# Optimization experiments

Hardware: AMD Instinct MI355X
Metric: run time of the kernel (lower is better)

## Reference

```python
import jax, jax.numpy as jnp
import numpy as np

NUM_USERS = 50000
NUM_ITEMS = 10000
NUM_SUPPORT = 5
INPUT_DIM = 512
OUTPUT_DIM = 500
NNZ = 400000


def setup_inputs() -> dict:
    key = jax.random.key(0)
    ks = jax.random.split(key, 6)
    x_u = jax.random.normal(ks[0], (NUM_USERS, INPUT_DIM), dtype=jnp.float32)
    x_v = jax.random.normal(ks[1], (NUM_ITEMS, INPUT_DIM), dtype=jnp.float32)
    # random-uniform-like weight init (weight_variable_random_uniform)
    weights_u = jax.random.normal(ks[2], (INPUT_DIM, OUTPUT_DIM), dtype=jnp.float32) * 0.05
    sup_vals = jax.random.uniform(ks[3], (NUM_SUPPORT, NNZ), dtype=jnp.float32)
    sup_rows = jax.random.randint(ks[4], (NUM_SUPPORT, NNZ), 0, NUM_USERS, dtype=jnp.int32)
    sup_cols = jax.random.randint(ks[5], (NUM_SUPPORT, NNZ), 0, NUM_ITEMS, dtype=jnp.int32)
    return {"x_u": x_u, "x_v": x_v, "weights_u": weights_u,
            "sup_vals": sup_vals, "sup_rows": sup_rows, "sup_cols": sup_cols}


def reference(x_u, x_v, weights_u, sup_vals, sup_rows, sup_cols):
    # share_user_item_weights=True -> weights_v is weights_u; dropout=0.0 -> identity.
    hidden = OUTPUT_DIM // NUM_SUPPORT  # 100
    supports_u, supports_v = [], []
    for i in range(NUM_SUPPORT):
        Wi = jax.lax.dynamic_slice_in_dim(weights_u, i * hidden, hidden, axis=1)
        tmp_u = x_u @ Wi  # [num_users, hidden]
        tmp_v = x_v @ Wi  # [num_items, hidden]
        vals = sup_vals[i][:, None]  # [nnz, 1]
        rows, cols = sup_rows[i], sup_cols[i]
        # support_i @ tmp_v  (sparse [U,I] times dense [I,h])
        su = jax.ops.segment_sum(vals * tmp_v[cols], rows, num_segments=NUM_USERS)
        # support_i^T @ tmp_u (sparse [I,U] times dense [U,h])
        sv = jax.ops.segment_sum(vals * tmp_u[rows], cols, num_segments=NUM_ITEMS)
        supports_u.append(su)
        supports_v.append(sv)
    z_u = jnp.concatenate(supports_u, axis=1)  # [num_users, output_dim]
    z_v = jnp.concatenate(supports_v, axis=1)  # [num_items, output_dim]
    return (jax.nn.relu(z_u), jax.nn.relu(z_v))
```

## Files before the change

### kernel.cpp

```cpp
#include <hip/hip_runtime.h>

#define NUM_USERS   50000
#define NUM_ITEMS   10000
#define NUM_SUPPORT 5
#define INPUT_DIM   512
#define OUTPUT_DIM  500
#define NPAD        512
#define HIDDEN      100
#define HPAD        128
#define NNZ         400000
#define NEDGE       (NUM_SUPPORT * NNZ)

#define CH_E        8192
#define NCHUNK      ((NEDGE + CH_E - 1) / CH_E)
#define NB_U        ((NUM_SUPPORT * NUM_USERS + 255) / 256)
#define NB_V        ((NUM_SUPPORT * NUM_ITEMS + 255) / 256)
#define HISTM_U_SZ  (NB_U * NCHUNK)
#define HISTM_U_ALIGN 239616
#define HISTM_V_SZ  (NB_V * NCHUNK)
#define HISTM_TOT   (HISTM_U_ALIGN + HISTM_V_SZ)

typedef unsigned int u32;
typedef unsigned short ushort_t;
typedef __attribute__((ext_vector_type(4))) float f32x4;
typedef __attribute__((ext_vector_type(8))) short bf16x8;

#define GLDS(g, l) __builtin_amdgcn_global_load_lds( \
    (const __attribute__((address_space(1))) unsigned int*)(g), \
    (__attribute__((address_space(3))) unsigned int*)(l), 16, 0, 0)

__device__ inline ushort_t bf16_rne(float f) {
    u32 u = __float_as_uint(f);
    u32 r = (u + 0x7FFFu + ((u >> 16) & 1u)) >> 16;
    return (ushort_t)r;
}
__device__ inline float bf16_lo_f32(u32 w) { return __uint_as_float(w << 16); }
__device__ inline float bf16_hi_f32(u32 w) { return __uint_as_float(w & 0xFFFF0000u); }

__global__ __launch_bounds__(256) void cvt_bf16_2(
    const float4* __restrict__ a, const float4* __restrict__ b,
    ushort4* __restrict__ oa, ushort4* __restrict__ ob, int na4, int nb4)
{
    int t = blockIdx.x * 256 + threadIdx.x;
    const float4* src;
    ushort4* dst;
    int idx;
    if (t < na4) { src = a; dst = oa; idx = t; }
    else { idx = t - na4; if (idx >= nb4) return; src = b; dst = ob; }
    float4 v = src[idx];
    ushort4 o;
    o.x = bf16_rne(v.x); o.y = bf16_rne(v.y);
    o.z = bf16_rne(v.z); o.w = bf16_rne(v.w);
    dst[idx] = o;
}

__global__ __launch_bounds__(256) void make_WbT(
    const float* __restrict__ W, ushort_t* __restrict__ WbT)
{
    int t = blockIdx.x * 256 + threadIdx.x;
    int n = t >> 9, k = t & 511;
    float v = (n < OUTPUT_DIM) ? W[k * OUTPUT_DIM + n] : 0.f;
    WbT[t] = bf16_rne(v);
}

#define BM 128
#define BN 128
#define BK 32

__global__ __launch_bounds__(256) void gemm_mfma_bf16(
    const ushort_t* __restrict__ A,
    const ushort_t* __restrict__ BT,
    ushort_t* __restrict__ Xp,
    int M)
{
    const int K = INPUT_DIM;
    __shared__ ushort_t As[BM * BK];
    __shared__ ushort_t Bs[BN * BK];

    const int tid  = threadIdx.x;
    const int wave = tid >> 6;
    const int lane = tid & 63;
    const int quad = lane >> 4;
    const int lr   = lane & 15;
    const int m0 = blockIdx.x * BM;
    const int n0 = blockIdx.y * BN;
    const int wm = (wave >> 1) * 64;
    const int wn = (wave & 1) * 64;

    f32x4 acc[4][4] = {};

    for (int k0 = 0; k0 < K; k0 += BK) {
        #pragma unroll
        for (int h = 0; h < 2; ++h) {
            int o   = tid * 16 + h * 4096;
            int row = o >> 6;
            int byt = o & 63;
            int gr  = m0 + row; if (gr >= M) gr = M - 1;
            GLDS((const char*)A + ((long long)gr * K + k0) * 2 + byt, (char*)As + o);
        }
        #pragma unroll
        for (int h = 0; h < 2; ++h) {
            int o   = tid * 16 + h * 4096;
            int row = o >> 6;
            int byt = o & 63;
            GLDS((const char*)BT + ((long long)(n0 + row) * K + k0) * 2 + byt, (char*)Bs + o);
        }
        asm volatile("s_waitcnt vmcnt(0)" ::: "memory");
        __syncthreads();

        bf16x8 af[4], bfr[4];
        #pragma unroll
        for (int tm = 0; tm < 4; ++tm)
            af[tm] = *(const bf16x8*)(As + (wm + tm * 16 + lr) * BK + quad * 8);
        #pragma unroll
        for (int tn = 0; tn < 4; ++tn)
            bfr[tn] = *(const bf16x8*)(Bs + (wn + tn * 16 + lr) * BK + quad * 8);
        #pragma unroll
        for (int tm = 0; tm < 4; ++tm)
            #pragma unroll
            for (int tn = 0; tn < 4; ++tn)
                acc[tm][tn] = __builtin_amdgcn_mfma_f32_16x16x32_bf16(
                    af[tm], bfr[tn], acc[tm][tn], 0, 0, 0);
        __syncthreads();
    }

    #pragma unroll
    for (int tm = 0; tm < 4; ++tm) {
        int rbase = m0 + wm + tm * 16 + quad * 4;
        #pragma unroll
        for (int tn = 0; tn < 4; ++tn) {
            int col = n0 + wn + tn * 16 + lr;
            if (col >= OUTPUT_DIM) continue;
            int seg = col / HIDDEN;
            int off = col - seg * HIDDEN;
            ushort_t* dst = Xp + (long long)seg * M * HPAD + off;
            #pragma unroll
            for (int g = 0; g < 4; ++g) {
                int row = rbase + g;
                if (row < M) dst[(long long)row * HPAD] = bf16_rne(acc[tm][tn][g]);
            }
        }
    }
}

__global__ __launch_bounds__(256) void scan1(u32* __restrict__ data, int n,
                                             u32* __restrict__ partials)
{
    __shared__ u32 sh[256];
    int t = threadIdx.x;
    int base = blockIdx.x * 1024 + t * 4;
    u32 x[4];
    #pragma unroll
    for (int k = 0; k < 4; ++k) {
        int idx = base + k;
        x[k] = (idx < n) ? data[idx] : 0u;
    }
    u32 tsum = x[0] + x[1] + x[2] + x[3];
    sh[t] = tsum;
    __syncthreads();
    for (int off = 1; off < 256; off <<= 1) {
        u32 v = (t >= off) ? sh[t - off] : 0u;
        __syncthreads();
        sh[t] += v;
        __syncthreads();
    }
    u32 run = (t > 0) ? sh[t - 1] : 0u;
    if (t == 255) partials[blockIdx.x] = sh[255];
    #pragma unroll
    for (int k = 0; k < 4; ++k) {
        int idx = base + k;
        if (idx < n) data[idx] = run;
        run += x[k];
    }
}

__global__ __launch_bounds__(512) void scan_partials(u32* __restrict__ partials, int n)
{
    __shared__ u32 sh[512];
    int t = threadIdx.x;
    u32 x = (t < n) ? partials[t] : 0u;
    sh[t] = x;
    __syncthreads();
    for (int off = 1; off < 512; off <<= 1) {
        u32 v = (t >= off) ? sh[t - off] : 0u;
        __syncthreads();
        sh[t] += v;
        __syncthreads();
    }
    if (t < n) partials[t] = (t > 0) ? sh[t - 1] : 0u;
}

__global__ __launch_bounds__(256) void scan_add(u32* __restrict__ data, int n,
                                                const u32* __restrict__ partials)
{
    int idx = blockIdx.x * 256 + threadIdx.x;
    if (idx >= n) return;
    u32 adj = (idx >= HISTM_U_ALIGN) ? (u32)NEDGE : 0u;
    data[idx] = data[idx] + partials[idx >> 10] - adj;
}

__global__ __launch_bounds__(256) void hist_uv(
    const int* __restrict__ rows, const int* __restrict__ cols,
    u32* __restrict__ histm_u, u32* __restrict__ histm_v)
{
    __shared__ u32 hu[NB_U];
    __shared__ u32 hv[NB_V];
    const int tid = threadIdx.x;
    const int c = blockIdx.x;
    if (c == 0)
        for (int z = HISTM_U_SZ + tid; z < HISTM_U_ALIGN; z += 256) histm_u[z] = 0u;
    for (int b = tid; b < NB_U; b += 256) hu[b] = 0u;
    for (int b = tid; b < NB_V; b += 256) hv[b] = 0u;
    __syncthreads();
    int base = c * CH_E;
    int end = base + CH_E; if (end > NEDGE) end = NEDGE;
    for (int e = base + tid; e < end; e += 256) {
        unsigned i = (unsigned)e / (unsigned)NNZ;
        u32 ku = i * (u32)NUM_USERS + (u32)rows[e];
        u32 kv = i * (u32)NUM_ITEMS + (u32)cols[e];
        atomicAdd(&hu[ku >> 8], 1u);
        atomicAdd(&hv[kv >> 8], 1u);
    }
    __syncthreads();
    for (int b = tid; b < NB_U; b += 256) histm_u[b * NCHUNK + c] = hu[b];
    for (int b = tid; b < NB_V; b += 256) histm_v[b * NCHUNK + c] = hv[b];
}

__global__ __launch_bounds__(256) void partition_uv(
    const int* __restrict__ rows, const int* __restrict__ cols,
    const float* __restrict__ vals,
    const u32* __restrict__ histm_u, const u32* __restrict__ histm_v,
    uint2* __restrict__ buf_u, uint2* __restrict__ buf_v)
{
    __shared__ u32 cu[NB_U];
    __shared__ u32 cv[NB_V];
    const int tid = threadIdx.x;
    const int c = blockIdx.x;
    for (int b = tid; b < NB_U; b += 256) cu[b] = histm_u[b * NCHUNK + c];
    for (int b = tid; b < NB_V; b += 256) cv[b] = histm_v[b * NCHUNK + c];
    __syncthreads();
    int base = c * CH_E;
    int end = base + CH_E; if (end > NEDGE) end = NEDGE;
    for (int e = base + tid; e < end; e += 256) {
        unsigned i = (unsigned)e / (unsigned)NNZ;
        int r = rows[e];
        int col = cols[e];
        u32 vb = __float_as_uint(vals[e]);
        u32 ku = i * (u32)NUM_USERS + (u32)r;
        u32 kv = i * (u32)NUM_ITEMS + (u32)col;
        u32 pu = atomicAdd(&cu[ku >> 8], 1u);
        uint2 eu; eu.x = vb; eu.y = (ku << 14) | (u32)col;
        buf_u[pu] = eu;
        u32 pv = atomicAdd(&cv[kv >> 8], 1u);
        uint2 ev; ev.x = vb; ev.y = (kv << 16) | (u32)r;
        buf_v[pv] = ev;
    }
}

template<int NROWS, int GSHIFT>
__device__ inline void bucket_body(
    int b, const uint2* __restrict__ buf, const u32* __restrict__ histm,
    u32* __restrict__ ptr, uint2* __restrict__ perm,
    u32* cnt, u32* scn)
{
    constexpr int NKEY = NUM_SUPPORT * NROWS;
    constexpr int NB = (NKEY + 255) / 256;
    const int tid = threadIdx.x;
    const u32 key0 = (u32)b << 8;
    const u32 start = histm[b * NCHUNK];
    const u32 bend  = (b + 1 < NB) ? histm[(b + 1) * NCHUNK] : (u32)NEDGE;
    if (b == 0 && tid == 0) ptr[NKEY] = (u32)NEDGE;
    cnt[tid] = 0u;
    __syncthreads();
    for (u32 j = start + tid; j < bend; j += 256) {
        u32 key = buf[j].y >> GSHIFT;
        atomicAdd(&cnt[key - key0], 1u);
    }
    __syncthreads();
    scn[tid] = cnt[tid];
    __syncthreads();
    for (int off = 1; off < 256; off <<= 1) {
        u32 v = (tid >= off) ? scn[tid - off] : 0u;
        __syncthreads();
        scn[tid] += v;
        __syncthreads();
    }
    u32 myoff = start + scn[tid] - cnt[tid];
    if (key0 + (u32)tid < (u32)NKEY) ptr[key0 + tid] = myoff;
    __syncthreads();
    cnt[tid] = myoff;
    __syncthreads();
    for (u32 j = start + tid; j < bend; j += 256) {
        uint2 q = buf[j];
        u32 key = q.y >> GSHIFT;
        u32 p = atomicAdd(&cnt[key - key0], 1u);
        uint2 out;
        out.x = q.x;
        out.y = q.y & ((1u << GSHIFT) - 1u);
        perm[p] = out;
    }
}

__global__ __launch_bounds__(256) void bucket_scatter_uv(
    const uint2* __restrict__ buf_u, const u32* __restrict__ histm_u,
    u32* __restrict__ ptr_u, uint2* __restrict__ perm_u,
    const uint2* __restrict__ buf_v, const u32* __restrict__ histm_v,
    u32* __restrict__ ptr_v, uint2* __restrict__ perm_v)
{
    __shared__ u32 cnt[256];
    __shared__ u32 scn[256];
    if (blockIdx.x < NB_U)
        bucket_body<NUM_USERS, 14>(blockIdx.x, buf_u, histm_u, ptr_u, perm_u, cnt, scn);
    else
        bucket_body<NUM_ITEMS, 16>(blockIdx.x - NB_U, buf_v, histm_v, ptr_v, perm_v, cnt, scn);
}

template<int NROWS>
__global__ __launch_bounds__(256) void spmm_pack4(
    const u32* __restrict__ ptr,
    const uint2* __restrict__ perm,
    const ushort_t* __restrict__ Xp,
    float* __restrict__ Z,
    int nsrc)
{
    constexpr int NKEY = NUM_SUPPORT * NROWS;
    int w = (int)((blockIdx.x * 256u + threadIdx.x) >> 6);
    w = __builtin_amdgcn_readfirstlane(w);
    if (w * 4 >= NKEY) return;
    const int lane = threadIdx.x & 63;
    const int g  = lane >> 4;
    const int sl = lane & 15;

    int key = w * 4 + g;
    int i = key / NROWS;
    int r = key - i * NROWS;
    u32 s = ptr[key];
    u32 e = ptr[key + 1];

    const ushort_t* Xs = Xp + (long long)i * nsrc * HPAD + sl * 8;

    u32 m = e - s;
    { u32 t = (u32)__shfl_xor((int)m, 16); m = m > t ? m : t; }
    { u32 t = (u32)__shfl_xor((int)m, 32); m = m > t ? m : t; }
    int iters = (int)((m + 3) >> 2);

    float a0 = 0.f, a1 = 0.f, a2 = 0.f, a3 = 0.f;
    float a4 = 0.f, a5 = 0.f, a6 = 0.f, a7 = 0.f;
    u32 k = s;
    for (int it = 0; it < iters; ++it) {
        bool p0 = k < e, p1 = (k + 1) < e, p2 = (k + 2) < e, p3 = (k + 3) < e;
        u32 j0 = p0 ? k : 0u;
        u32 j1 = p1 ? (k + 1) : 0u;
        u32 j2 = p2 ? (k + 2) : 0u;
        u32 j3 = p3 ? (k + 3) : 0u;
        uint2 q0 = perm[j0], q1 = perm[j1], q2 = perm[j2], q3 = perm[j3];
        float v0 = p0 ? __uint_as_float(q0.x) : 0.f;
        float v1 = p1 ? __uint_as_float(q1.x) : 0.f;
        float v2 = p2 ? __uint_as_float(q2.x) : 0.f;
        float v3 = p3 ? __uint_as_float(q3.x) : 0.f;
        uint4 w0 = *(const uint4*)(Xs + ((long long)q0.y << 7));
        uint4 w1 = *(const uint4*)(Xs + ((long long)q1.y << 7));
        uint4 w2 = *(const uint4*)(Xs + ((long long)q2.y << 7));
        uint4 w3 = *(const uint4*)(Xs + ((long long)q3.y << 7));
        a0 += v0 * bf16_lo_f32(w0.x) + v1 * bf16_lo_f32(w1.x)
            + v2 * bf16_lo_f32(w2.x) + v3 * bf16_lo_f32(w3.x);
        a1 += v0 * bf16_hi_f32(w0.x) + v1 * bf16_hi_f32(w1.x)
            + v2 * bf16_hi_f32(w2.x) + v3 * bf16_hi_f32(w3.x);
        a2 += v0 * bf16_lo_f32(w0.y) + v1 * bf16_lo_f32(w1.y)
            + v2 * bf16_lo_f32(w2.y) + v3 * bf16_lo_f32(w3.y);
        a3 += v0 * bf16_hi_f32(w0.y) + v1 * bf16_hi_f32(w1.y)
            + v2 * bf16_hi_f32(w2.y) + v3 * bf16_hi_f32(w3.y);
        a4 += v0 * bf16_lo_f32(w0.z) + v1 * bf16_lo_f32(w1.z)
            + v2 * bf16_lo_f32(w2.z) + v3 * bf16_lo_f32(w3.z);
        a5 += v0 * bf16_hi_f32(w0.z) + v1 * bf16_hi_f32(w1.z)
            + v2 * bf16_hi_f32(w2.z) + v3 * bf16_hi_f32(w3.z);
        a6 += v0 * bf16_lo_f32(w0.w) + v1 * bf16_lo_f32(w1.w)
            + v2 * bf16_lo_f32(w2.w) + v3 * bf16_lo_f32(w3.w);
        a7 += v0 * bf16_hi_f32(w0.w) + v1 * bf16_hi_f32(w1.w)
            + v2 * bf16_hi_f32(w2.w) + v3 * bf16_hi_f32(w3.w);
        k += 4;
    }

    if (sl < 13) {
        float* zp = Z + (long long)r * OUTPUT_DIM + i * HIDDEN + sl * 8;
        float4 o0;
        o0.x = a0 > 0.f ? a0 : 0.f;
        o0.y = a1 > 0.f ? a1 : 0.f;
        o0.z = a2 > 0.f ? a2 : 0.f;
        o0.w = a3 > 0.f ? a3 : 0.f;
        *(float4*)zp = o0;
        if (sl < 12) {
            float4 o1;
            o1.x = a4 > 0.f ? a4 : 0.f;
            o1.y = a5 > 0.f ? a5 : 0.f;
            o1.z = a6 > 0.f ? a6 : 0.f;
            o1.w = a7 > 0.f ? a7 : 0.f;
            *(float4*)(zp + 4) = o1;
        }
    }
}

#define TM 64
#define TN 64
#define TK 16

__global__ __launch_bounds__(256) void gemm_f32(
    const float* __restrict__ A, const float* __restrict__ B,
    float* __restrict__ C, int M, int N, int K, int ldc)
{
    __shared__ float Asl[TK][TM + 4];
    __shared__ float Bsl[TK][TN + 4];
    const int tid = threadIdx.x;
    const int tx  = tid & 15;
    const int ty  = tid >> 4;
    const int row0 = blockIdx.x * TM;
    const int col0 = blockIdx.y * TN;
    float acc[4][4] = {};
    for (int k0 = 0; k0 < K; k0 += TK) {
        #pragma unroll
        for (int it = 0; it < (TM * TK) / 256; ++it) {
            int idx = tid + it * 256;
            int m = idx >> 4, kk = idx & 15, gr = row0 + m;
            Asl[kk][m] = (gr < M) ? A[(long long)gr * K + (k0 + kk)] : 0.f;
        }
        #pragma unroll
        for (int it = 0; it < (TK * TN) / 256; ++it) {
            int idx = tid + it * 256;
            int kk = idx >> 6, n = idx & 63, gc = col0 + n;
            Bsl[kk][n] = (gc < N) ? B[(long long)(k0 + kk) * N + gc] : 0.f;
        }
        __syncthreads();
        #pragma unroll
        for (int kk = 0; kk < TK; ++kk) {
            float a[4], b[4];
            #pragma unroll
            for (int u = 0; u < 4; ++u) a[u] = Asl[kk][ty * 4 + u];
            #pragma unroll
            for (int v = 0; v < 4; ++v) b[v] = Bsl[kk][tx * 4 + v];
            #pragma unroll
            for (int u = 0; u < 4; ++u)
                #pragma unroll
                for (int v = 0; v < 4; ++v)
                    acc[u][v] += a[u] * b[v];
        }
        __syncthreads();
    }
    #pragma unroll
    for (int u = 0; u < 4; ++u) {
        int gr = row0 + ty * 4 + u;
        if (gr >= M) continue;
        #pragma unroll
        for (int v = 0; v < 4; ++v) {
            int gc = col0 + tx * 4 + v;
            if (gc < N) C[(long long)gr * ldc + gc] = acc[u][v];
        }
    }
}

__global__ __launch_bounds__(256) void scatter_edges(
    const float* __restrict__ sup_vals,
    const int*   __restrict__ sup_rows,
    const int*   __restrict__ sup_cols,
    const float* __restrict__ XU, const float* __restrict__ XV,
    float* __restrict__ z_u, float* __restrict__ z_v)
{
    const unsigned t = blockIdx.x * 256u + threadIdx.x;
    const unsigned total = (unsigned)NEDGE * HIDDEN;
    if (t >= total) return;
    const unsigned j  = t % HIDDEN;
    const unsigned eg = t / HIDDEN;
    const unsigned i  = eg / NNZ;
    const float val = sup_vals[eg];
    const int   r   = sup_rows[eg];
    const int   c   = sup_cols[eg];
    const int   colOff = i * HIDDEN + j;
    atomicAdd(&z_u[(long long)r * OUTPUT_DIM + colOff],
              val * XV[(long long)c * NPAD + colOff]);
    atomicAdd(&z_v[(long long)c * OUTPUT_DIM + colOff],
              val * XU[(long long)r * NPAD + colOff]);
}

__global__ __launch_bounds__(256) void relu_inplace(float4* __restrict__ p, int n4)
{
    int t = blockIdx.x * 256 + threadIdx.x;
    if (t >= n4) return;
    float4 v = p[t];
    v.x = v.x > 0.f ? v.x : 0.f;
    v.y = v.y > 0.f ? v.y : 0.f;
    v.z = v.z > 0.f ? v.z : 0.f;
    v.w = v.w > 0.f ? v.w : 0.f;
    p[t] = v;
}

extern "C" void kernel_launch(void* const* d_in, const int* in_sizes, int n_in,
                              void* d_out, int out_size, void* d_ws, size_t ws_size,
                              hipStream_t stream)
{
    const float* x_u      = (const float*)d_in[0];
    const float* x_v      = (const float*)d_in[1];
    const float* W        = (const float*)d_in[2];
    const float* sup_vals = (const float*)d_in[3];
    const int*   sup_rows = (const int*)d_in[4];
    const int*   sup_cols = (const int*)d_in[5];

    float* z_u = (float*)d_out;
    float* z_v = z_u + (long long)NUM_USERS * OUTPUT_DIM;

    const long long NU = (long long)NUM_USERS * 512;
    const long long NV = (long long)NUM_ITEMS * 512;
    const long long PU = (long long)NUM_SUPPORT * NUM_USERS * HPAD;
    const long long PV = (long long)NUM_SUPPORT * NUM_ITEMS * HPAD;
    const int NRU = NUM_SUPPORT * NUM_USERS;
    const int NRV = NUM_SUPPORT * NUM_ITEMS;

    ushort_t* Xp_u  = (ushort_t*)d_ws;
    ushort_t* Xp_v  = Xp_u + PU;
    ushort_t* xu_in = Xp_v + PV;
    ushort_t* xv_in = xu_in + NU;
    ushort_t* WbT   = xv_in + NV;
    u32* row_ptr_u  = (u32*)(WbT + 512 * 512);
    u32* col_ptr_v  = row_ptr_u + (NRU + 1);
    u32* partials   = col_ptr_v + (NRV + 1);
    size_t need_full = ((char*)(partials + 512)) - ((char*)d_ws);

    uint2* buf_v    = (uint2*)xu_in;
    u32*   histm_u  = (u32*)(buf_v + NEDGE);
    u32*   histm_v  = histm_u + HISTM_U_ALIGN;
    uint2* perm_u   = (uint2*)(histm_v + HISTM_V_SZ);
    uint2* perm_v   = perm_u + NEDGE;
    uint2* buf_u    = (uint2*)z_u;

    dim3 blk(256);

    if (ws_size >= need_full) {
        {
            int na4 = (int)(NU / 4), nb4 = (int)(NV / 4);
            cvt_bf16_2<<<(na4 + nb4 + 255) / 256, blk, 0, stream>>>(
                (const float4*)x_u, (const float4*)x_v,
                (ushort4*)xu_in, (ushort4*)xv_in, na4, nb4);
        }
        make_WbT<<<(512 * 512) / 256, blk, 0, stream>>>(W, WbT);
        gemm_mfma_bf16<<<dim3((NUM_USERS + BM - 1) / BM, 512 / BN), blk, 0, stream>>>(
            xu_in, WbT, Xp_u, NUM_USERS);
        gemm_mfma_bf16<<<dim3((NUM_ITEMS + BM - 1) / BM, 512 / BN), blk, 0, stream>>>(
            xv_in, WbT, Xp_v, NUM_ITEMS);

        hist_uv<<<NCHUNK, blk, 0, stream>>>(sup_rows, sup_cols, histm_u, histm_v);

        {
            int nb = (HISTM_TOT + 1023) / 1024;
            scan1<<<nb, blk, 0, stream>>>(histm_u, HISTM_TOT, partials);
            scan_partials<<<1, dim3(512), 0, stream>>>(partials, nb);
            scan_add<<<(HISTM_TOT + 255) / 256, blk, 0, stream>>>(
                histm_u, HISTM_TOT, partials);
        }

        partition_uv<<<NCHUNK, blk, 0, stream>>>(
            sup_rows, sup_cols, sup_vals, histm_u, histm_v, buf_u, buf_v);

        bucket_scatter_uv<<<NB_U + NB_V, blk, 0, stream>>>(
            buf_u, histm_u, row_ptr_u, perm_u,
            buf_v, histm_v, col_ptr_v, perm_v);

        spmm_pack4<NUM_USERS><<<((NRU / 4) * 64) / 256, blk, 0, stream>>>(
            row_ptr_u, perm_u, Xp_v, z_u, NUM_ITEMS);
        spmm_pack4<NUM_ITEMS><<<((NRV / 4) * 64) / 256, blk, 0, stream>>>(
            col_ptr_v, perm_v, Xp_u, z_v, NUM_USERS);
    } else {
        float* XU = (float*)d_ws;
        float* XV = XU + (long long)NUM_USERS * NPAD;
        gemm_f32<<<dim3((NUM_USERS + TM - 1) / TM, (OUTPUT_DIM + TN - 1) / TN),
                   blk, 0, stream>>>(x_u, W, XU, NUM_USERS, OUTPUT_DIM, INPUT_DIM, NPAD);
        gemm_f32<<<dim3((NUM_ITEMS + TM - 1) / TM, (OUTPUT_DIM + TN - 1) / TN),
                   blk, 0, stream>>>(x_v, W, XV, NUM_ITEMS, OUTPUT_DIM, INPUT_DIM, NPAD);
        hipMemsetAsync(d_out, 0, (size_t)out_size * sizeof(float), stream);
        unsigned total = (unsigned)NEDGE * HIDDEN;
        scatter_edges<<<(total + 255u) / 256u, blk, 0, stream>>>(
            sup_vals, sup_rows, sup_cols, XU, XV, z_u, z_v);
        int n4 = out_size / 4;
        relu_inplace<<<(n4 + 255) / 256, blk, 0, stream>>>((float4*)d_out, n4);
    }
}
```

Baseline: 519.2 us.

## Sort item-side edges by source-user quarter and swizzle SpMM blocks across XCDs

```diff
diff --git a/kernel.cpp b/kernel.cpp
--- a/kernel.cpp
+++ b/kernel.cpp
@@ -14,10 +14,11 @@
 #define CH_E        8192
 #define NCHUNK      ((NEDGE + CH_E - 1) / CH_E)
 #define NB_U        ((NUM_SUPPORT * NUM_USERS + 255) / 256)
-#define NB_V        ((NUM_SUPPORT * NUM_ITEMS + 255) / 256)
+#define NKEY_V2     (NUM_SUPPORT * NUM_ITEMS * 4)
+#define NB_V2       ((NKEY_V2 + 255) / 256)
 #define HISTM_U_SZ  (NB_U * NCHUNK)
 #define HISTM_U_ALIGN 239616
-#define HISTM_V_SZ  (NB_V * NCHUNK)
+#define HISTM_V_SZ  (NB_V2 * NCHUNK)
 #define HISTM_TOT   (HISTM_U_ALIGN + HISTM_V_SZ)
 
 typedef unsigned int u32;
@@ -36,6 +37,17 @@
 }
 __device__ inline float bf16_lo_f32(u32 w) { return __uint_as_float(w << 16); }
 __device__ inline float bf16_hi_f32(u32 w) { return __uint_as_float(w & 0xFFFF0000u); }
+
+__device__ inline u32 rb3(u32 r) {
+    return (r >= 12500u ? 1u : 0u) + (r >= 25000u ? 1u : 0u) + (r >= 37500u ? 1u : 0u);
+}
+
+__device__ inline int xcd_swizzle(int bid, int nwg) {
+    int q = nwg >> 3, rmd = nwg & 7;
+    int xcd = bid & 7, idx = bid >> 3;
+    int base = (xcd < rmd) ? xcd * (q + 1) : rmd * (q + 1) + (xcd - rmd) * q;
+    return base + idx;
+}
 
 __global__ __launch_bounds__(256) void cvt_bf16_2(
     const float4* __restrict__ a, const float4* __restrict__ b,
@@ -204,26 +216,27 @@
     u32* __restrict__ histm_u, u32* __restrict__ histm_v)
 {
     __shared__ u32 hu[NB_U];
-    __shared__ u32 hv[NB_V];
+    __shared__ u32 hv[NB_V2];
     const int tid = threadIdx.x;
     const int c = blockIdx.x;
     if (c == 0)
         for (int z = HISTM_U_SZ + tid; z < HISTM_U_ALIGN; z += 256) histm_u[z] = 0u;
     for (int b = tid; b < NB_U; b += 256) hu[b] = 0u;
-    for (int b = tid; b < NB_V; b += 256) hv[b] = 0u;
+    for (int b = tid; b < NB_V2; b += 256) hv[b] = 0u;
     __syncthreads();
     int base = c * CH_E;
     int end = base + CH_E; if (end > NEDGE) end = NEDGE;
     for (int e = base + tid; e < end; e += 256) {
         unsigned i = (unsigned)e / (unsigned)NNZ;
-        u32 ku = i * (u32)NUM_USERS + (u32)rows[e];
-        u32 kv = i * (u32)NUM_ITEMS + (u32)cols[e];
+        u32 r = (u32)rows[e];
+        u32 ku = i * (u32)NUM_USERS + r;
+        u32 knew = (i * (u32)NUM_ITEMS + (u32)cols[e]) * 4u + rb3(r);
         atomicAdd(&hu[ku >> 8], 1u);
-        atomicAdd(&hv[kv >> 8], 1u);
+        atomicAdd(&hv[knew >> 8], 1u);
     }
     __syncthreads();
     for (int b = tid; b < NB_U; b += 256) histm_u[b * NCHUNK + c] = hu[b];
-    for (int b = tid; b < NB_V; b += 256) histm_v[b * NCHUNK + c] = hv[b];
+    for (int b = tid; b < NB_V2; b += 256) histm_v[b * NCHUNK + c] = hv[b];
 }
 
 __global__ __launch_bounds__(256) void partition_uv(
@@ -233,38 +246,38 @@
     uint2* __restrict__ buf_u, uint2* __restrict__ buf_v)
 {
     __shared__ u32 cu[NB_U];
-    __shared__ u32 cv[NB_V];
+    __shared__ u32 cv[NB_V2];
     const int tid = threadIdx.x;
     const int c = blockIdx.x;
     for (int b = tid; b < NB_U; b += 256) cu[b] = histm_u[b * NCHUNK + c];
-    for (int b = tid; b < NB_V; b += 256) cv[b] = histm_v[b * NCHUNK + c];
+    for (int b = tid; b < NB_V2; b += 256) cv[b] = histm_v[b * NCHUNK + c];
     __syncthreads();
     int base = c * CH_E;
     int end = base + CH_E; if (end > NEDGE) end = NEDGE;
     for (int e = base + tid; e < end; e += 256) {
         unsigned i = (unsigned)e / (unsigned)NNZ;
-        int r = rows[e];
-        int col = cols[e];
+        u32 r = (u32)rows[e];
+        u32 col = (u32)cols[e];
         u32 vb = __float_as_uint(vals[e]);
-        u32 ku = i * (u32)NUM_USERS + (u32)r;
-        u32 kv = i * (u32)NUM_ITEMS + (u32)col;
+        u32 ku = i * (u32)NUM_USERS + r;
+        u32 kv16 = i * (u32)NUM_ITEMS + col;
+        u32 knew = kv16 * 4u + rb3(r);
         u32 pu = atomicAdd(&cu[ku >> 8], 1u);
-        uint2 eu; eu.x = vb; eu.y = (ku << 14) | (u32)col;
+        uint2 eu; eu.x = vb; eu.y = (ku << 14) | col;
         buf_u[pu] = eu;
-        u32 pv = atomicAdd(&cv[kv >> 8], 1u);
-        uint2 ev; ev.x = vb; ev.y = (kv << 16) | (u32)r;
+        u32 pv = atomicAdd(&cv[knew >> 8], 1u);
+        uint2 ev; ev.x = vb; ev.y = (kv16 << 16) | r;
         buf_v[pv] = ev;
     }
 }
 
-template<int NROWS, int GSHIFT>
-__device__ inline void bucket_body(
+__device__ inline void bucket_body_u(
     int b, const uint2* __restrict__ buf, const u32* __restrict__ histm,
     u32* __restrict__ ptr, uint2* __restrict__ perm,
     u32* cnt, u32* scn)
 {
-    constexpr int NKEY = NUM_SUPPORT * NROWS;
-    constexpr int NB = (NKEY + 255) / 256;
+    constexpr int NKEY = NUM_SUPPORT * NUM_USERS;
+    constexpr int NB = NB_U;
     const int tid = threadIdx.x;
     const u32 key0 = (u32)b << 8;
     const u32 start = histm[b * NCHUNK];
@@ -273,7 +286,7 @@
     cnt[tid] = 0u;
     __syncthreads();
     for (u32 j = start + tid; j < bend; j += 256) {
-        u32 key = buf[j].y >> GSHIFT;
+        u32 key = buf[j].y >> 14;
         atomicAdd(&cnt[key - key0], 1u);
     }
     __syncthreads();
@@ -292,11 +305,55 @@
     __syncthreads();
     for (u32 j = start + tid; j < bend; j += 256) {
         uint2 q = buf[j];
-        u32 key = q.y >> GSHIFT;
+        u32 key = q.y >> 14;
         u32 p = atomicAdd(&cnt[key - key0], 1u);
         uint2 out;
         out.x = q.x;
-        out.y = q.y & ((1u << GSHIFT) - 1u);
+        out.y = q.y & 0x3FFFu;
+        perm[p] = out;
+    }
+}
+
+__device__ inline void bucket_body_v(
+    int b, const uint2* __restrict__ buf, const u32* __restrict__ histm,
+    u32* __restrict__ ptr, uint2* __restrict__ perm,
+    u32* cnt, u32* scn)
+{
+    constexpr int NKEY = NKEY_V2;
+    constexpr int NB = NB_V2;
+    const int tid = threadIdx.x;
+    const u32 key0 = (u32)b << 8;
+    const u32 start = histm[b * NCHUNK];
+    const u32 bend  = (b + 1 < NB) ? histm[(b + 1) * NCHUNK] : (u32)NEDGE;
+    if (b == 0 && tid == 0) ptr[NKEY] = (u32)NEDGE;
+    cnt[tid] = 0u;
+    __syncthreads();
+    for (u32 j = start + tid; j < bend; j += 256) {
+        u32 y = buf[j].y;
+        u32 key = (y >> 16) * 4u + rb3(y & 0xFFFFu);
+        atomicAdd(&cnt[key - key0], 1u);
+    }
+    __syncthreads();
+    scn[tid] = cnt[tid];
+    __syncthreads();
+    for (int off = 1; off < 256; off <<= 1) {
+        u32 v = (tid >= off) ? scn[tid - off] : 0u;
+        __syncthreads();
+        scn[tid] += v;
+        __syncthreads();
+    }
+    u32 myoff = start + scn[tid] - cnt[tid];
+    if (key0 + (u32)tid < (u32)NKEY) ptr[key0 + tid] = myoff;
+    __syncthreads();
+    cnt[tid] = myoff;
+    __syncthreads();
+    for (u32 j = start + tid; j < bend; j += 256) {
+        uint2 q = buf[j];
+        u32 key = (q.y >> 16) * 4u + rb3(q.y & 0xFFFFu);
+        u32 p = atomicAdd(&cnt[key - key0], 1u);
+        uint2 out;
+        out.x = q.x;
+        out.y = q.y & 0xFFFFu;
         perm[p] = out;
     }
 }
@@ -310,12 +367,12 @@
     __shared__ u32 cnt[256];
     __shared__ u32 scn[256];
     if (blockIdx.x < NB_U)
-        bucket_body<NUM_USERS, 14>(blockIdx.x, buf_u, histm_u, ptr_u, perm_u, cnt, scn);
+        bucket_body_u(blockIdx.x, buf_u, histm_u, ptr_u, perm_u, cnt, scn);
     else
-        bucket_body<NUM_ITEMS, 16>(blockIdx.x - NB_U, buf_v, histm_v, ptr_v, perm_v, cnt, scn);
-}
-
-template<int NROWS>
+        bucket_body_v(blockIdx.x - NB_U, buf_v, histm_v, ptr_v, perm_v, cnt, scn);
+}
+
+template<int NROWS, int PSTR>
 __global__ __launch_bounds__(256) void spmm_pack4(
     const u32* __restrict__ ptr,
     const uint2* __restrict__ perm,
@@ -324,7 +381,8 @@
     int nsrc)
 {
     constexpr int NKEY = NUM_SUPPORT * NROWS;
-    int w = (int)((blockIdx.x * 256u + threadIdx.x) >> 6);
+    int bid = xcd_swizzle(blockIdx.x, gridDim.x);
+    int w = bid * 4 + (int)(threadIdx.x >> 6);
     w = __builtin_amdgcn_readfirstlane(w);
     if (w * 4 >= NKEY) return;
     const int lane = threadIdx.x & 63;
@@ -334,8 +392,8 @@
     int key = w * 4 + g;
     int i = key / NROWS;
     int r = key - i * NROWS;
-    u32 s = ptr[key];
-    u32 e = ptr[key + 1];
+    u32 s = ptr[key * PSTR];
+    u32 e = ptr[(key + 1) * PSTR];
 
     const ushort_t* Xs = Xp + (long long)i * nsrc * HPAD + sl * 8;
 
@@ -520,7 +578,7 @@
     ushort_t* WbT   = xv_in + NV;
     u32* row_ptr_u  = (u32*)(WbT + 512 * 512);
     u32* col_ptr_v  = row_ptr_u + (NRU + 1);
-    u32* partials   = col_ptr_v + (NRV + 1);
+    u32* partials   = col_ptr_v + (NKEY_V2 + 1);
     size_t need_full = ((char*)(partials + 512)) - ((char*)d_ws);
 
     uint2* buf_v    = (uint2*)xu_in;
@@ -558,13 +616,13 @@
         partition_uv<<<NCHUNK, blk, 0, stream>>>(
             sup_rows, sup_cols, sup_vals, histm_u, histm_v, buf_u, buf_v);
 
-        bucket_scatter_uv<<<NB_U + NB_V, blk, 0, stream>>>(
+        bucket_scatter_uv<<<NB_U + NB_V2, blk, 0, stream>>>(
             buf_u, histm_u, row_ptr_u, perm_u,
             buf_v, histm_v, col_ptr_v, perm_v);
 
-        spmm_pack4<NUM_USERS><<<((NRU / 4) * 64) / 256, blk, 0, stream>>>(
+        spmm_pack4<NUM_USERS, 1><<<((NRU / 4) * 64) / 256, blk, 0, stream>>>(
             row_ptr_u, perm_u, Xp_v, z_u, NUM_ITEMS);
-        spmm_pack4<NUM_ITEMS><<<((NRV / 4) * 64) / 256, blk, 0, stream>>>(
+        spmm_pack4<NUM_ITEMS, 4><<<((NRV / 4) * 64) / 256, blk, 0, stream>>>(
             col_ptr_v, perm_v, Xp_u, z_v, NUM_USERS);
     } else {
         float* XU = (float*)d_ws;
```

After: 513.7 us. Within noise of the previous version (-1.1%).
